# Performance work log

Hardware: AMD Instinct MI355X
Metric: run time of the kernel (lower is better)

The kernel has to match this reference:

```python
import jax, jax.numpy as jnp
import numpy as np

W_PROFILE, W_PLANFORM, W_MEAN = 0.5, 0.3, 0.2
CELL_SIZE = 10.0
EPS = 1e-08


def _kernels():
    sobel_x = np.array([[-1, 0, 1], [-2, 0, 2], [-1, 0, 1]], np.float32) / 8.0
    sobel_y = np.array([[-1, -2, -1], [0, 0, 0], [1, 2, 1]], np.float32) / 8.0
    k_xx = np.array([[1, -2, 1], [1, -2, 1], [1, -2, 1]], np.float32) / 3.0
    k_yy = np.array([[1, 1, 1], [-2, -2, -2], [1, 1, 1]], np.float32) / 3.0
    k_xy = np.array([[-1, 0, 1], [0, 0, 0], [1, 0, -1]], np.float32) / 4.0
    # stack into one [5,1,3,3] OIHW kernel -> single fused conv for all 5 stencils
    return jnp.asarray(np.stack([sobel_x, sobel_y, k_xx, k_xy, k_yy])[:, None])

_K = _kernels()


def _curvatures(dem):
    # dem: [B,1,H,W] -> derivatives p,q,r,s,t each [B,1,H,W]
    d = jax.lax.conv_general_dilated(dem, _K, window_strides=(1, 1), padding='SAME',
                                     dimension_numbers=('NCHW', 'OIHW', 'NCHW'))
    p = d[:, 0:1] / CELL_SIZE
    q = d[:, 1:2] / CELL_SIZE
    r = d[:, 2:3] / CELL_SIZE ** 2
    s = d[:, 3:4] / CELL_SIZE ** 2
    t = d[:, 4:5] / CELL_SIZE ** 2
    p2, q2, pq = p * p, q * q, p * q
    denom1 = p2 + q2
    denom2 = (1 + denom1) ** 1.5
    profile = (r * p2 + 2 * s * pq + t * q2) / (denom1 * jnp.sqrt(1 + denom1) + EPS)
    planform = (r * q2 - 2 * s * pq + t * p2) / (denom1 ** 1.5 + EPS)
    mean = ((1 + q2) * r - 2 * pq * s + (1 + p2) * t) / (2 * denom2 + EPS)
    flat = denom1 < EPS
    profile = jnp.where(flat, 0.0, profile)
    planform = jnp.where(flat, 0.0, planform)
    return profile, planform, mean


def setup_inputs() -> dict:
    key = jax.random.key(0)
    k1, k2 = jax.random.split(key)
    shape = (16, 1, 1024, 1024)
    return {
        'pred': jax.random.normal(k1, shape, dtype=jnp.float32),
        'target': jax.random.normal(k2, shape, dtype=jnp.float32),
    }


def reference(pred, target):
    pp, pl, pm = _curvatures(pred)
    tp, tl, tm = _curvatures(target)
    loss_profile = jnp.mean(jnp.abs(pp - tp))
    loss_planform = jnp.mean(jnp.abs(pl - tl))
    loss_mean = jnp.mean(jnp.abs(pm - tm))
    return W_PROFILE * loss_profile + W_PLANFORM * loss_planform + W_MEAN * loss_mean
```

## Files before the change

kernel.cpp:

```cpp
#include <hip/hip_runtime.h>
#include <math.h>


constexpr int IMG_B = 16;
constexpr int IMG_H = 1024;
constexpr int IMG_W = 1024;
constexpr int ROWS  = 16;
constexpr int BLOCK = 256;
constexpr int TILES_X = IMG_W / BLOCK;
constexpr int TILES_Y = IMG_H / ROWS;
constexpr int NBLOCKS = IMG_B * TILES_Y * TILES_X;
constexpr float EPS = 1e-8f;

constexpr float A2 = 1.0f / 6400.0f;
constexpr float Bc = 1.0f / 300.0f;
constexpr float C2 = 1.0f / 200.0f;

typedef float f2v __attribute__((ext_vector_type(2)));

__device__ __forceinline__ f2v pk_fma(f2v a, f2v b, f2v c) {
    return __builtin_elementwise_fma(a, b, c);
}

struct Rowv { f2v hx, hs, rs; };

__device__ __forceinline__ void curv_pair(const Rowv& a, const Rowv& b, const Rowv& c,
                                          f2v& prof, f2v& plan, f2v& mean2)
{
    const f2v A2f = {A2, A2}, Bcf = {Bc, Bc}, C2f = {C2, C2};
    const f2v m3  = {-3.0f, -3.0f}, two = {2.0f, 2.0f};
    const f2v epsf = {EPS, EPS};

    const f2v gx  = pk_fma(two, b.hx, a.hx + c.hx);
    const f2v gy  = c.hs - a.hs;
    const f2v tot = (a.rs + c.rs) + b.rs;
    const f2v H   = (a.hs + c.hs) + b.hs;
    const f2v rxx = pk_fma(m3, H - tot, tot);
    const f2v tyy = pk_fma(m3, b.rs, tot);
    const f2v sxy = a.hx - c.hx;

    const f2v gx2 = gx * gx, gy2 = gy * gy, gxgy = gx * gy;
    const f2v g2  = gx2 + gy2;
    const f2v d1  = A2f * g2;
    const f2v od  = d1 + f2v{1.0f, 1.0f};

    f2v rsq_od, sq_d1;
    rsq_od.x = __builtin_amdgcn_rsqf(od.x);
    rsq_od.y = __builtin_amdgcn_rsqf(od.y);
    sq_d1.x  = __builtin_amdgcn_sqrtf(d1.x);
    sq_d1.y  = __builtin_amdgcn_sqrtf(d1.y);
    const f2v sq_od = od * rsq_od;

    const f2v h1    = pk_fma(tyy, gy2, rxx * gx2);
    const f2v h3    = pk_fma(tyy, gx2, rxx * gy2);
    const f2v h2c   = C2f * (sxy * gxgy);
    const f2v nprof = A2f * pk_fma(Bcf, h1,  h2c);
    const f2v nplan = A2f * pk_fma(Bcf, h3, -h2c);
    const f2v mnum  = pk_fma(Bcf, rxx + tyy, nplan);

    const f2v den_p = pk_fma(d1, sq_od, epsf);
    const f2v den_l = pk_fma(d1, sq_d1, epsf);
    const f2v plprod = den_p * den_l;
    f2v rcpPL;
    rcpPL.x = __builtin_amdgcn_rcpf(plprod.x);
    rcpPL.y = __builtin_amdgcn_rcpf(plprod.y);

    prof  = (nprof * den_l) * rcpPL;
    plan  = (nplan * den_p) * rcpPL;
    mean2 = mnum * ((rsq_od * rsq_od) * rsq_od);
    prof.x = (d1.x < EPS) ? 0.0f : prof.x;
    prof.y = (d1.y < EPS) ? 0.0f : prof.y;
    plan.x = (d1.x < EPS) ? 0.0f : plan.x;
    plan.y = (d1.y < EPS) ? 0.0f : plan.y;
}

__global__ __launch_bounds__(BLOCK, 4) void curv_loss_main(
    const float* __restrict__ pred, const float* __restrict__ targ,
    float* __restrict__ blocksums)
{
    const int tid = threadIdx.x;
    const int b   = blockIdx.x;
    const int tx  = b & (TILES_X - 1);
    const int ty  = (b >> 2) & (TILES_Y - 1);
    const int img = b >> 8;
    const int y0  = ty * ROWS;
    const int x   = tx * BLOCK + tid;

    const size_t ibase = (size_t)img * (size_t)(IMG_H * IMG_W);
    const char* __restrict__ Pc = (const char*)(pred + ibase);
    const char* __restrict__ Tc = (const char*)(targ + ibase);

    const bool xm = (x > 0);
    const bool xp = (x < IMG_W - 1);
    const int eL = (x + (xm ? -1 : 0)) << 2;
    const int eC = x << 2;
    const int eR = (x + (xp ? +1 : 0)) << 2;

    auto prep = [&](int y, Rowv& o) {
        if ((unsigned)y < (unsigned)IMG_H) {
            const int vo = y << 12;
            const float pl = *(const float*)(Pc + vo + eL);
            const float tl = *(const float*)(Tc + vo + eL);
            const float pc = *(const float*)(Pc + vo + eC);
            const float tc = *(const float*)(Tc + vo + eC);
            const float pr = *(const float*)(Pc + vo + eR);
            const float tr = *(const float*)(Tc + vo + eR);
            const f2v w0 = {xm ? pl : 0.0f, xm ? tl : 0.0f};
            const f2v w1 = {pc, tc};
            const f2v w2 = {xp ? pr : 0.0f, xp ? tr : 0.0f};
            const f2v e = w0 + w2;
            o.hx = w2 - w0;
            o.hs = pk_fma(f2v{2.0f, 2.0f}, w1, e);
            o.rs = e + w1;
        } else {
            o.hx = f2v{0.0f, 0.0f}; o.hs = f2v{0.0f, 0.0f}; o.rs = f2v{0.0f, 0.0f};
        }
    };

    Rowv w[3];
    prep(y0 - 1, w[0]);
    prep(y0,     w[1]);

    float acc = 0.0f;
#pragma unroll
    for (int i = 0; i < ROWS; ++i) {
        const int ia = i % 3, ib = (i + 1) % 3, ic = (i + 2) % 3;
        prep(y0 + i + 1, w[ic]);
        f2v prof, plan, mean2;
        curv_pair(w[ia], w[ib], w[ic], prof, plan, mean2);
        acc = fmaf(0.5f, fabsf(prof.x  - prof.y),  acc);
        acc = fmaf(0.3f, fabsf(plan.x  - plan.y),  acc);
        acc = fmaf(0.1f, fabsf(mean2.x - mean2.y), acc);
    }

#pragma unroll
    for (int off = 32; off > 0; off >>= 1) acc += __shfl_down(acc, off, 64);
    __shared__ float ws[BLOCK / 64];
    const int lane = tid & 63, wid = tid >> 6;
    if (lane == 0) ws[wid] = acc;
    __syncthreads();
    if (tid == 0)
        blocksums[b] = (ws[0] + ws[1]) + (ws[2] + ws[3]);
}

__global__ __launch_bounds__(BLOCK) void curv_loss_final(
    const float* __restrict__ blocksums, float* __restrict__ out)
{
    const int tid = threadIdx.x;
    float v = 0.0f;
#pragma unroll
    for (int i = 0; i < NBLOCKS / BLOCK; ++i) v += blocksums[i * BLOCK + tid];
#pragma unroll
    for (int off = 32; off > 0; off >>= 1) v += __shfl_down(v, off, 64);
    __shared__ float ws[BLOCK / 64];
    const int lane = tid & 63, wid = tid >> 6;
    if (lane == 0) ws[wid] = v;
    __syncthreads();
    if (tid == 0) {
        const float tot = (ws[0] + ws[1]) + (ws[2] + ws[3]);
        out[0] = tot * (1.0f / (float)(IMG_B * IMG_H * IMG_W));
    }
}

extern "C" void kernel_launch(void* const* d_in, const int* in_sizes, int n_in,
                              void* d_out, int out_size, void* d_ws, size_t ws_size,
                              hipStream_t stream)
{
    const float* pred = (const float*)d_in[0];
    const float* targ = (const float*)d_in[1];
    float* out = (float*)d_out;
    float* blocksums = (float*)d_ws;

    curv_loss_main<<<NBLOCKS, BLOCK, 0, stream>>>(pred, targ, blocksums);
    curv_loss_final<<<1, BLOCK, 0, stream>>>(blocksums, out);
}
```

Before: 152.9 us.

## Use wavefront shuffles for horizontal neighbors instead of redundant global loads

```diff
diff --git a/kernel.cpp b/kernel.cpp
--- a/kernel.cpp
+++ b/kernel.cpp
@@ -7,9 +7,13 @@
 constexpr int IMG_W = 1024;
 constexpr int ROWS  = 16;
 constexpr int BLOCK = 256;
-constexpr int TILES_X = IMG_W / BLOCK;
+constexpr int WCOLS = 62;
+constexpr int TCOLS = WCOLS * 4;
+constexpr int TILES_X = (IMG_W + TCOLS - 1) / TCOLS;
 constexpr int TILES_Y = IMG_H / ROWS;
 constexpr int NBLOCKS = IMG_B * TILES_Y * TILES_X;
+constexpr int TILES_X7 = IMG_W / BLOCK;
+constexpr int NBLOCKS7 = IMG_B * TILES_Y * TILES_X7;
 constexpr float EPS = 1e-8f;
 
 constexpr float A2 = 1.0f / 6400.0f;
@@ -74,13 +78,88 @@
     plan.y = (d1.y < EPS) ? 0.0f : plan.y;
 }
 
-__global__ __launch_bounds__(BLOCK, 4) void curv_loss_main(
+__global__ __launch_bounds__(BLOCK) void curv_loss_main_shfl(
     const float* __restrict__ pred, const float* __restrict__ targ,
     float* __restrict__ blocksums)
 {
     const int tid = threadIdx.x;
     const int b   = blockIdx.x;
-    const int tx  = b & (TILES_X - 1);
+    const int tx  = b % TILES_X;
+    const int r2  = b / TILES_X;
+    const int ty  = r2 & (TILES_Y - 1);
+    const int img = r2 >> 6;
+    const int y0  = ty * ROWS;
+    const int wv  = tid >> 6, l = tid & 63;
+    const int cl  = tx * TCOLS + wv * WCOLS + l - 1;
+    const bool validC = (unsigned)cl < (unsigned)IMG_W;
+    const int  eC = (validC ? cl : (cl < 0 ? 0 : IMG_W - 1)) << 2;
+    const bool outv = (l >= 1) && (l <= WCOLS) && validC;
+    const float W05 = outv ? 0.5f : 0.0f;
+    const float W03 = outv ? 0.3f : 0.0f;
+    const float W01 = outv ? 0.1f : 0.0f;
+
+    const size_t ibase = (size_t)img * (size_t)(IMG_H * IMG_W);
+    const char* __restrict__ Pc = (const char*)(pred + ibase);
+    const char* __restrict__ Tc = (const char*)(targ + ibase);
+
+    float acc = 0.0f;
+    if (__ballot(outv) != 0ULL) {
+        auto prep = [&](int y, Rowv& o) {
+            if ((unsigned)y < (unsigned)IMG_H) {
+                const int vo = y << 12;
+                float pc = *(const float*)(Pc + vo + eC);
+                float tc = *(const float*)(Tc + vo + eC);
+                pc = validC ? pc : 0.0f;
+                tc = validC ? tc : 0.0f;
+                const float p0 = __shfl_up(pc, 1u, 64);
+                const float t0 = __shfl_up(tc, 1u, 64);
+                const float p2 = __shfl_down(pc, 1u, 64);
+                const float t2 = __shfl_down(tc, 1u, 64);
+                const f2v w0 = {p0, t0};
+                const f2v w1 = {pc, tc};
+                const f2v w2 = {p2, t2};
+                const f2v e = w0 + w2;
+                o.hx = w2 - w0;
+                o.hs = pk_fma(f2v{2.0f, 2.0f}, w1, e);
+                o.rs = e + w1;
+            } else {
+                o.hx = f2v{0.0f, 0.0f}; o.hs = f2v{0.0f, 0.0f}; o.rs = f2v{0.0f, 0.0f};
+            }
+        };
+
+        Rowv w[3];
+        prep(y0 - 1, w[0]);
+        prep(y0,     w[1]);
+
+#pragma unroll
+        for (int i = 0; i < ROWS; ++i) {
+            const int ia = i % 3, ib = (i + 1) % 3, ic = (i + 2) % 3;
+            prep(y0 + i + 1, w[ic]);
+            f2v prof, plan, mean2;
+            curv_pair(w[ia], w[ib], w[ic], prof, plan, mean2);
+            acc = fmaf(W05, fabsf(prof.x  - prof.y),  acc);
+            acc = fmaf(W03, fabsf(plan.x  - plan.y),  acc);
+            acc = fmaf(W01, fabsf(mean2.x - mean2.y), acc);
+        }
+    }
+
+#pragma unroll
+    for (int off = 32; off > 0; off >>= 1) acc += __shfl_down(acc, off, 64);
+    __shared__ float ws[BLOCK / 64];
+    const int lane = tid & 63, wid = tid >> 6;
+    if (lane == 0) ws[wid] = acc;
+    __syncthreads();
+    if (tid == 0)
+        blocksums[b] = (ws[0] + ws[1]) + (ws[2] + ws[3]);
+}
+
+__global__ __launch_bounds__(BLOCK) void curv_loss_main_r7(
+    const float* __restrict__ pred, const float* __restrict__ targ,
+    float* __restrict__ blocksums)
+{
+    const int tid = threadIdx.x;
+    const int b   = blockIdx.x;
+    const int tx  = b & (TILES_X7 - 1);
     const int ty  = (b >> 2) & (TILES_Y - 1);
     const int img = b >> 8;
     const int y0  = ty * ROWS;
@@ -144,12 +223,11 @@
 }
 
 __global__ __launch_bounds__(BLOCK) void curv_loss_final(
-    const float* __restrict__ blocksums, float* __restrict__ out)
+    const float* __restrict__ blocksums, int n, float* __restrict__ out)
 {
     const int tid = threadIdx.x;
     float v = 0.0f;
-#pragma unroll
-    for (int i = 0; i < NBLOCKS / BLOCK; ++i) v += blocksums[i * BLOCK + tid];
+    for (int i = tid; i < n; i += BLOCK) v += blocksums[i];
 #pragma unroll
     for (int off = 32; off > 0; off >>= 1) v += __shfl_down(v, off, 64);
     __shared__ float ws[BLOCK / 64];
@@ -171,6 +249,11 @@
     float* out = (float*)d_out;
     float* blocksums = (float*)d_ws;
 
-    curv_loss_main<<<NBLOCKS, BLOCK, 0, stream>>>(pred, targ, blocksums);
-    curv_loss_final<<<1, BLOCK, 0, stream>>>(blocksums, out);
-}
+    if (ws_size >= (size_t)NBLOCKS * sizeof(float)) {
+        curv_loss_main_shfl<<<NBLOCKS, BLOCK, 0, stream>>>(pred, targ, blocksums);
+        curv_loss_final<<<1, BLOCK, 0, stream>>>(blocksums, NBLOCKS, out);
+    } else {
+        curv_loss_main_r7<<<NBLOCKS7, BLOCK, 0, stream>>>(pred, targ, blocksums);
+        curv_loss_final<<<1, BLOCK, 0, stream>>>(blocksums, NBLOCKS7, out);
+    }
+}
```

New measurement: 164.8 us. 7.8% more time.
